# Kernel optimization log

Hardware: AMD Instinct MI355X
Metric: run time of the kernel (lower is better)

## Reference

```python
import jax, jax.numpy as jnp
import numpy as np

KER = 3          # CausalPool1d kernel
PAD_VAL = 1e-8   # left-pad value
K = 3            # harmonic_num
H = 4200         # rows of integral matrix
F = 321          # frequency bins


def setup_inputs() -> dict:
    key = jax.random.key(0)
    k1, k2, k3 = jax.random.split(key, 3)
    mag = jax.random.uniform(k1, (8, 2, F, 1000), dtype=jnp.float32)          # B,C,F,T (magnitude >= 0)
    integral_m = jax.random.normal(k2, (H, F), dtype=jnp.float32)             # buffer integral_m (squeezed)
    harmonic_loc = jax.random.normal(k3, (H, F), dtype=jnp.float32)           # buffer harmonic_loc (squeezed)
    return {"mag": mag, "integral_m": integral_m, "harmonic_loc": harmonic_loc, "freq_dim": F}


def reference(mag, integral_m, harmonic_loc, freq_dim):
    # harmonic_nominee: (B,C,H,T) = integral_m @ mag
    nominee = jnp.einsum('hf,bcft->bcht', integral_m, mag)
    # topk over the H axis (torch dim=-2); lax.top_k works on last axis -> move H last
    _, pos = jax.lax.top_k(jnp.moveaxis(nominee, 2, -1), K)  # (B,C,T,K), descending like torch
    pos = jnp.moveaxis(pos, -1, 2).astype(jnp.float32)       # (B,C,K,T)
    # CausalPool1d: left-pad (KER-1) with 1e-8, avg over window KER, stride 1 (vectorized over K)
    xp = jnp.pad(pos, ((0, 0), (0, 0), (0, 0), (KER - 1, 0)), constant_values=PAD_VAL)
    T = pos.shape[-1]
    choose = ((xp[..., 0:T] + xp[..., 1:T + 1] + xp[..., 2:T + 2]) / KER).astype(jnp.int32)  # (B,C,K,T)
    # gather harmonic_loc rows and accumulate over the K harmonics
    gathered = harmonic_loc[choose]          # (B,C,K,T,F)
    summed = gathered.sum(axis=2)            # (B,C,T,F)
    # (B,C,F,T) threshold mask, matching torch's (x > 0).float()
    out = (jnp.swapaxes(summed, -1, -2) > 0).astype(jnp.float32)
    return out
```

## Files before the change

### kernel.cpp

```cpp
#include <hip/hip_runtime.h>
#include <math.h>

#define F_DIM 321
#define H_DIM 4200
#define T_DIM 1000
#define NBC   16
#define KTOP  3
#define PADV  1e-8f

#define BM 128
#define BN 128
#define BK 16
#define LDA 16
#define LDB 128
#define NHT 33
#define NKT 20

typedef float v4f __attribute__((ext_vector_type(4)));
typedef __attribute__((address_space(3))) uint32_t lds_u32;
typedef const __attribute__((address_space(1))) uint32_t glb_u32;

__device__ __forceinline__ void ins3(float v, int i,
                                     float& v0, float& v1, float& v2,
                                     int& i0, int& i1, int& i2) {
  if (v > v0)      { v2 = v1; i2 = i1; v1 = v0; i1 = i0; v0 = v; i0 = i; }
  else if (v > v1) { v2 = v1; i2 = i1; v1 = v;  i1 = i; }
  else if (v > v2) { v2 = v;  i2 = i; }
}

__global__ __launch_bounds__(256)
void hi_k1_gemm_top3(const float* __restrict__ mag,
                     const float* __restrict__ im,
                     float* __restrict__ wv, int* __restrict__ wi,
                     int nsplit) {
  const int tid = threadIdx.x;
  const int tx = tid & 15;
  const int ty = tid >> 4;
  const int wv_ = tid >> 6;
  const int lam = tid & 63;
  const int t0 = blockIdx.x * BN;
  const int bc = blockIdx.y;
  const int sp = blockIdx.z;
  const int ht_begin = (sp * NHT) / nsplit;
  const int ht_end   = ((sp + 1) * NHT) / nsplit;
  const int nht = ht_end - ht_begin;
  const int NT = nht * NKT;
  const int row0 = ty * 8;
  const int xsw = (ty & 3) << 2;

  __shared__ __align__(16) float As[2][BM * LDA];
  __shared__ __align__(16) float Bs[2][BK * LDB];
  __shared__ float mv[4 * BN * KTOP];
  __shared__ int   mi[4 * BN * KTOP];

  const float* magbc = mag + (size_t)bc * F_DIM * T_DIM;

  auto stageA = [&](int buf, int nh0, int nk0) {
#pragma unroll
    for (int i = 0; i < 8; ++i) {
      int row = wv_ * 32 + i * 4 + (lam >> 4);
      int gh = nh0 + row;
      gh = (gh < H_DIM) ? gh : (H_DIM - 1);
      int key = ((row >> 3) & 3) << 2;
      const float* src = im + (size_t)gh * F_DIM + nk0 + ((lam & 15) ^ key);
      __builtin_amdgcn_global_load_lds(
          (glb_u32*)src,
          (lds_u32*)&As[buf][(wv_ * 32 + i * 4) * LDA], 4, 0, 0);
    }
  };
  auto stageB = [&](int buf, int nk0) {
#pragma unroll
    for (int i = 0; i < 2; ++i) {
      int kr = wv_ * 4 + i * 2 + (lam >> 5);
      const float* src = magbc + (size_t)(nk0 + kr) * T_DIM + t0 + (lam & 31) * 4;
      __builtin_amdgcn_global_load_lds(
          (glb_u32*)src,
          (lds_u32*)&Bs[buf][(wv_ * 4 + i * 2) * LDB], 16, 0, 0);
    }
  };
  auto nh0_of = [&](int i) { return (ht_begin + i / NKT) * BM; };
  auto nk0_of = [&](int i) { return (i % NKT) * BK; };

  float gv0 = -INFINITY, gv1 = -INFINITY, gv2 = -INFINITY;
  int   gi0 = 0, gi1 = 0, gi2 = 0;

  stageA(0, nh0_of(0), nk0_of(0)); stageB(0, nk0_of(0));
  stageA(1, nh0_of(1), nk0_of(1)); stageB(1, nk0_of(1));
  asm volatile("s_waitcnt vmcnt(10)" ::: "memory");
  __builtin_amdgcn_s_barrier();
  __builtin_amdgcn_sched_barrier(0);

  int cur = 0;
  for (int ht = 0; ht < nht; ++ht) {
    const int h0 = (ht_begin + ht) * BM;
    float acc[8][8];
#pragma unroll
    for (int r = 0; r < 8; ++r)
#pragma unroll
      for (int c = 0; c < 8; ++c) acc[r][c] = 0.f;

    for (int kt = 0; kt < NKT; ++kt) {
      const int i = ht * NKT + kt;

#pragma unroll 1
      for (int g = 0; g < 4; ++g) {
        v4f Bv[8];
#pragma unroll
        for (int kk = 0; kk < 4; ++kk) {
          Bv[kk * 2]     = *(const v4f*)(&Bs[cur][(g * 4 + kk) * LDB + tx * 4]);
          Bv[kk * 2 + 1] = *(const v4f*)(&Bs[cur][(g * 4 + kk) * LDB + 64 + tx * 4]);
        }
#pragma unroll
        for (int r = 0; r < 8; ++r) {
          const v4f Ar = *(const v4f*)(&As[cur][(row0 + r) * LDA + ((g * 4) ^ xsw)]);
#pragma unroll
          for (int kk = 0; kk < 4; ++kk)
#pragma unroll
            for (int c = 0; c < 4; ++c) {
              acc[r][c]     = fmaf(Ar[kk], Bv[kk * 2][c],     acc[r][c]);
              acc[r][c + 4] = fmaf(Ar[kk], Bv[kk * 2 + 1][c], acc[r][c + 4]);
            }
        }
      }

      asm volatile("" ::: "memory");
      __builtin_amdgcn_s_barrier();
      __builtin_amdgcn_sched_barrier(0);

      if (i + 2 < NT) {
        stageA(cur, nh0_of(i + 2), nk0_of(i + 2));
        stageB(cur, nk0_of(i + 2));
        asm volatile("s_waitcnt vmcnt(10)" ::: "memory");
      } else {
        asm volatile("s_waitcnt vmcnt(0)" ::: "memory");
      }
      asm volatile("" ::: "memory");
      __builtin_amdgcn_s_barrier();
      __builtin_amdgcn_sched_barrier(0);
      cur ^= 1;
    }

    {
      float bt[8];
#pragma unroll
      for (int c = 0; c < 8; ++c) {
        int gt = t0 + ((c < 4) ? (tx * 4 + c) : (64 + tx * 4 + c - 4));
        bt[c] = (gt < T_DIM) ? magbc[(size_t)(F_DIM - 1) * T_DIM + gt] : 0.f;
      }
#pragma unroll
      for (int r = 0; r < 8; ++r) {
        int gh = h0 + row0 + r;
        float a = (gh < H_DIM) ? im[(size_t)gh * F_DIM + (F_DIM - 1)] : 0.f;
#pragma unroll
        for (int c = 0; c < 8; ++c) acc[r][c] = fmaf(a, bt[c], acc[r][c]);
      }
    }

#pragma unroll
    for (int c = 0; c < 8; ++c) {
      const int col = (c < 4) ? (tx * 4 + c) : (64 + tx * 4 + c - 4);
      float v0 = -INFINITY, v1 = -INFINITY, v2 = -INFINITY;
      int   i0 = 0, i1 = 0, i2 = 0;
#pragma unroll
      for (int r = 0; r < 8; ++r) {
        int gh = h0 + row0 + r;
        float v = (gh < H_DIM) ? acc[r][c] : -INFINITY;
        ins3(v, gh, v0, v1, v2, i0, i1, i2);
      }
#pragma unroll
      for (int s = 0; s < 2; ++s) {
        const int off = 16 << s;
        float ov0 = __shfl_down(v0, off);
        float ov1 = __shfl_down(v1, off);
        float ov2 = __shfl_down(v2, off);
        int   oi0 = __shfl_down(i0, off);
        int   oi1 = __shfl_down(i1, off);
        int   oi2 = __shfl_down(i2, off);
        ins3(ov0, oi0, v0, v1, v2, i0, i1, i2);
        ins3(ov1, oi1, v0, v1, v2, i0, i1, i2);
        ins3(ov2, oi2, v0, v1, v2, i0, i1, i2);
      }
      if ((ty & 3) == 0) {
        mv[(wv_ * BN + col) * 3 + 0] = v0;
        mv[(wv_ * BN + col) * 3 + 1] = v1;
        mv[(wv_ * BN + col) * 3 + 2] = v2;
        mi[(wv_ * BN + col) * 3 + 0] = i0;
        mi[(wv_ * BN + col) * 3 + 1] = i1;
        mi[(wv_ * BN + col) * 3 + 2] = i2;
      }
    }
    __syncthreads();
    if (tid < BN) {
#pragma unroll
      for (int w = 0; w < 4; ++w)
#pragma unroll
        for (int j = 0; j < 3; ++j) {
          float v = mv[(w * BN + tid) * 3 + j];
          int   i = mi[(w * BN + tid) * 3 + j];
          ins3(v, i, gv0, gv1, gv2, gi0, gi1, gi2);
        }
    }
    __syncthreads();
  }

  if (tid < BN) {
    int t = t0 + tid;
    if (t < T_DIM) {
      size_t base = ((size_t)(bc * nsplit + sp) * KTOP) * T_DIM + t;
      wv[base]             = gv0;
      wv[base + T_DIM]     = gv1;
      wv[base + 2 * T_DIM] = gv2;
      wi[base]             = gi0;
      wi[base + T_DIM]     = gi1;
      wi[base + 2 * T_DIM] = gi2;
    }
  }
}

__global__ __launch_bounds__(256, 4)
void hi_k3_pool_gather(const float* __restrict__ wv, const int* __restrict__ wi,
                       const float* __restrict__ hl, float* __restrict__ out,
                       int nsplit) {
  const int tid = threadIdx.x;
  const int t0 = blockIdx.x * 64;
  const int bc = blockIdx.y;

  __shared__ float pos_lds[66 * KTOP];
  __shared__ int   rows[64 * KTOP];
  __shared__ float S[64 * 65];

  if (tid < 66) {
    int t = t0 - 2 + tid;
    float p0 = PADV, p1 = PADV, p2 = PADV;
    if (t >= 0 && t < T_DIM) {
      float v0 = -INFINITY, v1 = -INFINITY, v2 = -INFINITY;
      int i0 = 0, i1 = 0, i2 = 0;
      for (int sp = 0; sp < nsplit; ++sp)
        for (int j = 0; j < KTOP; ++j) {
          size_t idx = ((size_t)(bc * nsplit + sp) * KTOP + j) * T_DIM + t;
          ins3(wv[idx], wi[idx], v0, v1, v2, i0, i1, i2);
        }
      p0 = (float)i0; p1 = (float)i1; p2 = (float)i2;
    }
    pos_lds[tid * KTOP + 0] = p0;
    pos_lds[tid * KTOP + 1] = p1;
    pos_lds[tid * KTOP + 2] = p2;
  }
  __syncthreads();
  if (tid < 64) {
#pragma unroll
    for (int k = 0; k < KTOP; ++k) {
      float s = (pos_lds[tid * KTOP + k] + pos_lds[(tid + 1) * KTOP + k])
                + pos_lds[(tid + 2) * KTOP + k];
      rows[tid * KTOP + k] = (int)(s / 3.0f);
    }
  }
  __syncthreads();

  const int w = tid >> 6, lane = tid & 63;
  for (int fc = 0; fc < 6; ++fc) {
    const int f0 = fc * 64;
    for (int i = 0; i < 16; ++i) {
      int tl = w * 16 + i;
      int r0 = rows[tl * KTOP + 0];
      int r1 = rows[tl * KTOP + 1];
      int r2 = rows[tl * KTOP + 2];
      int f = f0 + lane;
      float s = 0.f;
      if (f < F_DIM)
        s = (hl[(size_t)r0 * F_DIM + f] + hl[(size_t)r1 * F_DIM + f])
            + hl[(size_t)r2 * F_DIM + f];
      S[tl * 65 + lane] = s;
    }
    __syncthreads();
#pragma unroll
    for (int i = 0; i < 16; ++i) {
      int e = tid + 256 * i;
      int fl = e >> 6, tl = e & 63;
      int f = f0 + fl, t = t0 + tl;
      if (f < F_DIM && t < T_DIM)
        out[((size_t)bc * F_DIM + f) * T_DIM + t] = (S[tl * 65 + fl] > 0.f) ? 1.f : 0.f;
    }
    __syncthreads();
  }
}

extern "C" void kernel_launch(void* const* d_in, const int* in_sizes, int n_in,
                              void* d_out, int out_size, void* d_ws, size_t ws_size,
                              hipStream_t stream) {
  const float* mag = (const float*)d_in[0];
  const float* im  = (const float*)d_in[1];
  const float* hl  = (const float*)d_in[2];
  float* out = (float*)d_out;

  int nsplit = (ws_size >= (size_t)NBC * 8 * KTOP * T_DIM * 8) ? 8 : 4;
  float* wv = (float*)d_ws;
  int*   wi = (int*)d_ws + (size_t)NBC * nsplit * KTOP * T_DIM;

  dim3 g1((T_DIM + BN - 1) / BN, NBC, nsplit);
  hipLaunchKernelGGL(hi_k1_gemm_top3, g1, dim3(256), 0, stream, mag, im, wv, wi, nsplit);

  dim3 g3((T_DIM + 63) / 64, NBC);
  hipLaunchKernelGGL(hi_k3_pool_gather, g3, dim3(256), 0, stream, wv, wi, hl, out, nsplit);
}
```

Baseline: 1.026 ms.

## Restructure top-3 GEMM to stream integral rows via scalar loads with wider column tiles

Each block now handles 32 rows of integral_m and 256 time columns, and each wave owns 8 rows. The A operand is no longer staged through LDS: each wave reads its rows with wave-uniform (readfirstlane) addresses, so they can become scalar loads feeding the FMAs directly. Only the mag tile is double-buffered through LDS, and the top-3 reduction drops its cross-lane shuffles because each lane already covers all rows of its columns. The H split now goes up to 32 when the workspace allows, which adds more partial results for the second kernel to merge. The change relies on scalar-cache hit rates and on whether unaligned scalar loads are efficient.

```diff
diff --git a/kernel.cpp b/kernel.cpp
--- a/kernel.cpp
+++ b/kernel.cpp
@@ -8,13 +8,12 @@
 #define KTOP  3
 #define PADV  1e-8f
 
-#define BM 128
-#define BN 128
+#define BM 32
+#define BN 256
 #define BK 16
-#define LDA 16
-#define LDB 128
-#define NHT 33
+#define NRT 132
 #define NKT 20
+#define NTT 4
 
 typedef float v4f __attribute__((ext_vector_type(4)));
 typedef __attribute__((address_space(3))) uint32_t lds_u32;
@@ -33,104 +32,88 @@
                      const float* __restrict__ im,
                      float* __restrict__ wv, int* __restrict__ wi,
                      int nsplit) {
-  const int tid = threadIdx.x;
-  const int tx = tid & 15;
-  const int ty = tid >> 4;
-  const int wv_ = tid >> 6;
-  const int lam = tid & 63;
+  const int tid  = threadIdx.x;
+  const int lane = tid & 63;
+  const int w    = tid >> 6;
   const int t0 = blockIdx.x * BN;
   const int bc = blockIdx.y;
   const int sp = blockIdx.z;
-  const int ht_begin = (sp * NHT) / nsplit;
-  const int ht_end   = ((sp + 1) * NHT) / nsplit;
-  const int nht = ht_end - ht_begin;
-  const int NT = nht * NKT;
-  const int row0 = ty * 8;
-  const int xsw = (ty & 3) << 2;
-
-  __shared__ __align__(16) float As[2][BM * LDA];
-  __shared__ __align__(16) float Bs[2][BK * LDB];
-  __shared__ float mv[4 * BN * KTOP];
-  __shared__ int   mi[4 * BN * KTOP];
+  const int rt_begin = (sp * NRT) / nsplit;
+  const int rt_end   = ((sp + 1) * NRT) / nsplit;
+
+  __shared__ __align__(16) float Bs[2][BK * BN];
+  float* mv = (float*)&Bs[0][0];
+  int*   mi = (int*)(&Bs[0][0] + 4 * BN * KTOP);
 
   const float* magbc = mag + (size_t)bc * F_DIM * T_DIM;
 
-  auto stageA = [&](int buf, int nh0, int nk0) {
-#pragma unroll
-    for (int i = 0; i < 8; ++i) {
-      int row = wv_ * 32 + i * 4 + (lam >> 4);
-      int gh = nh0 + row;
-      gh = (gh < H_DIM) ? gh : (H_DIM - 1);
-      int key = ((row >> 3) & 3) << 2;
-      const float* src = im + (size_t)gh * F_DIM + nk0 + ((lam & 15) ^ key);
+  auto stageB = [&](int buf, int k0) {
+#pragma unroll
+    for (int i = 0; i < 4; ++i) {
+      int kr = w * 4 + i;
+      const float* src = magbc + (size_t)(k0 + kr) * T_DIM + t0 + lane * 4;
       __builtin_amdgcn_global_load_lds(
-          (glb_u32*)src,
-          (lds_u32*)&As[buf][(wv_ * 32 + i * 4) * LDA], 4, 0, 0);
+          (glb_u32*)src, (lds_u32*)&Bs[buf][kr * BN], 16, 0, 0);
     }
   };
-  auto stageB = [&](int buf, int nk0) {
-#pragma unroll
-    for (int i = 0; i < 2; ++i) {
-      int kr = wv_ * 4 + i * 2 + (lam >> 5);
-      const float* src = magbc + (size_t)(nk0 + kr) * T_DIM + t0 + (lam & 31) * 4;
-      __builtin_amdgcn_global_load_lds(
-          (glb_u32*)src,
-          (lds_u32*)&Bs[buf][(wv_ * 4 + i * 2) * LDB], 16, 0, 0);
-    }
-  };
-  auto nh0_of = [&](int i) { return (ht_begin + i / NKT) * BM; };
-  auto nk0_of = [&](int i) { return (i % NKT) * BK; };
 
   float gv0 = -INFINITY, gv1 = -INFINITY, gv2 = -INFINITY;
   int   gi0 = 0, gi1 = 0, gi2 = 0;
 
-  stageA(0, nh0_of(0), nk0_of(0)); stageB(0, nk0_of(0));
-  stageA(1, nh0_of(1), nk0_of(1)); stageB(1, nk0_of(1));
-  asm volatile("s_waitcnt vmcnt(10)" ::: "memory");
-  __builtin_amdgcn_s_barrier();
-  __builtin_amdgcn_sched_barrier(0);
-
-  int cur = 0;
-  for (int ht = 0; ht < nht; ++ht) {
-    const int h0 = (ht_begin + ht) * BM;
-    float acc[8][8];
+  for (int rt = rt_begin; rt < rt_end; ++rt) {
+    const int h0 = rt * BM;
+    int ab[8];
+#pragma unroll
+    for (int r = 0; r < 8; ++r) {
+      int gh = h0 + w * 8 + r;
+      if (gh >= H_DIM) gh = H_DIM - 1;
+      ab[r] = __builtin_amdgcn_readfirstlane(gh * F_DIM);
+    }
+
+    float acc[8][4];
 #pragma unroll
     for (int r = 0; r < 8; ++r)
 #pragma unroll
-      for (int c = 0; c < 8; ++c) acc[r][c] = 0.f;
-
+      for (int c = 0; c < 4; ++c) acc[r][c] = 0.f;
+
+    stageB(0, 0);
+    stageB(1, BK);
+    asm volatile("s_waitcnt vmcnt(4)" ::: "memory");
+    __builtin_amdgcn_s_barrier();
+    __builtin_amdgcn_sched_barrier(0);
+
+    int cur = 0;
     for (int kt = 0; kt < NKT; ++kt) {
-      const int i = ht * NKT + kt;
-
-#pragma unroll 1
+      const int k0 = kt * BK;
+#pragma unroll 2
       for (int g = 0; g < 4; ++g) {
-        v4f Bv[8];
-#pragma unroll
-        for (int kk = 0; kk < 4; ++kk) {
-          Bv[kk * 2]     = *(const v4f*)(&Bs[cur][(g * 4 + kk) * LDB + tx * 4]);
-          Bv[kk * 2 + 1] = *(const v4f*)(&Bs[cur][(g * 4 + kk) * LDB + 64 + tx * 4]);
-        }
-#pragma unroll
-        for (int r = 0; r < 8; ++r) {
-          const v4f Ar = *(const v4f*)(&As[cur][(row0 + r) * LDA + ((g * 4) ^ xsw)]);
-#pragma unroll
-          for (int kk = 0; kk < 4; ++kk)
-#pragma unroll
-            for (int c = 0; c < 4; ++c) {
-              acc[r][c]     = fmaf(Ar[kk], Bv[kk * 2][c],     acc[r][c]);
-              acc[r][c + 4] = fmaf(Ar[kk], Bv[kk * 2 + 1][c], acc[r][c + 4]);
-            }
-        }
+        const int kk0 = k0 + g * 4;
+        float a[8][4];
+#pragma unroll
+        for (int r = 0; r < 8; ++r)
+#pragma unroll
+          for (int q = 0; q < 4; ++q)
+            a[r][q] = im[ab[r] + kk0 + q];
+        v4f Bv[4];
+#pragma unroll
+        for (int q = 0; q < 4; ++q)
+          Bv[q] = *(const v4f*)(&Bs[cur][(g * 4 + q) * BN + lane * 4]);
+#pragma unroll
+        for (int r = 0; r < 8; ++r)
+#pragma unroll
+          for (int q = 0; q < 4; ++q)
+#pragma unroll
+            for (int c = 0; c < 4; ++c)
+              acc[r][c] = fmaf(a[r][q], Bv[q][c], acc[r][c]);
       }
 
       asm volatile("" ::: "memory");
       __builtin_amdgcn_s_barrier();
       __builtin_amdgcn_sched_barrier(0);
 
-      if (i + 2 < NT) {
-        stageA(cur, nh0_of(i + 2), nk0_of(i + 2));
-        stageB(cur, nk0_of(i + 2));
-        asm volatile("s_waitcnt vmcnt(10)" ::: "memory");
+      if (kt + 2 < NKT) {
+        stageB(cur, (kt + 2) * BK);
+        asm volatile("s_waitcnt vmcnt(4)" ::: "memory");
       } else {
         asm volatile("s_waitcnt vmcnt(0)" ::: "memory");
       }
@@ -141,69 +124,54 @@
     }
 
     {
-      float bt[8];
-#pragma unroll
-      for (int c = 0; c < 8; ++c) {
-        int gt = t0 + ((c < 4) ? (tx * 4 + c) : (64 + tx * 4 + c - 4));
+      float bt[4];
+#pragma unroll
+      for (int c = 0; c < 4; ++c) {
+        int gt = t0 + lane * 4 + c;
         bt[c] = (gt < T_DIM) ? magbc[(size_t)(F_DIM - 1) * T_DIM + gt] : 0.f;
       }
 #pragma unroll
       for (int r = 0; r < 8; ++r) {
-        int gh = h0 + row0 + r;
-        float a = (gh < H_DIM) ? im[(size_t)gh * F_DIM + (F_DIM - 1)] : 0.f;
-#pragma unroll
-        for (int c = 0; c < 8; ++c) acc[r][c] = fmaf(a, bt[c], acc[r][c]);
-      }
-    }
-
-#pragma unroll
-    for (int c = 0; c < 8; ++c) {
-      const int col = (c < 4) ? (tx * 4 + c) : (64 + tx * 4 + c - 4);
+        float av = im[ab[r] + (F_DIM - 1)];
+#pragma unroll
+        for (int c = 0; c < 4; ++c) acc[r][c] = fmaf(av, bt[c], acc[r][c]);
+      }
+    }
+
+#pragma unroll
+    for (int c = 0; c < 4; ++c) {
+      const int col = lane * 4 + c;
       float v0 = -INFINITY, v1 = -INFINITY, v2 = -INFINITY;
       int   i0 = 0, i1 = 0, i2 = 0;
 #pragma unroll
       for (int r = 0; r < 8; ++r) {
-        int gh = h0 + row0 + r;
+        int gh = h0 + w * 8 + r;
         float v = (gh < H_DIM) ? acc[r][c] : -INFINITY;
         ins3(v, gh, v0, v1, v2, i0, i1, i2);
       }
-#pragma unroll
-      for (int s = 0; s < 2; ++s) {
-        const int off = 16 << s;
-        float ov0 = __shfl_down(v0, off);
-        float ov1 = __shfl_down(v1, off);
-        float ov2 = __shfl_down(v2, off);
-        int   oi0 = __shfl_down(i0, off);
-        int   oi1 = __shfl_down(i1, off);
-        int   oi2 = __shfl_down(i2, off);
-        ins3(ov0, oi0, v0, v1, v2, i0, i1, i2);
-        ins3(ov1, oi1, v0, v1, v2, i0, i1, i2);
-        ins3(ov2, oi2, v0, v1, v2, i0, i1, i2);
-      }
-      if ((ty & 3) == 0) {
-        mv[(wv_ * BN + col) * 3 + 0] = v0;
-        mv[(wv_ * BN + col) * 3 + 1] = v1;
-        mv[(wv_ * BN + col) * 3 + 2] = v2;
-        mi[(wv_ * BN + col) * 3 + 0] = i0;
-        mi[(wv_ * BN + col) * 3 + 1] = i1;
-        mi[(wv_ * BN + col) * 3 + 2] = i2;
-      }
-    }
-    __syncthreads();
-    if (tid < BN) {
-#pragma unroll
-      for (int w = 0; w < 4; ++w)
+      mv[(w * BN + col) * 3 + 0] = v0;
+      mv[(w * BN + col) * 3 + 1] = v1;
+      mv[(w * BN + col) * 3 + 2] = v2;
+      mi[(w * BN + col) * 3 + 0] = i0;
+      mi[(w * BN + col) * 3 + 1] = i1;
+      mi[(w * BN + col) * 3 + 2] = i2;
+    }
+    __syncthreads();
+    {
+      const int col = tid;
+#pragma unroll
+      for (int ww = 0; ww < 4; ++ww)
 #pragma unroll
         for (int j = 0; j < 3; ++j) {
-          float v = mv[(w * BN + tid) * 3 + j];
-          int   i = mi[(w * BN + tid) * 3 + j];
+          float v = mv[(ww * BN + col) * 3 + j];
+          int   i = mi[(ww * BN + col) * 3 + j];
           ins3(v, i, gv0, gv1, gv2, gi0, gi1, gi2);
         }
     }
     __syncthreads();
   }
 
-  if (tid < BN) {
+  {
     int t = t0 + tid;
     if (t < T_DIM) {
       size_t base = ((size_t)(bc * nsplit + sp) * KTOP) * T_DIM + t;
@@ -293,11 +261,13 @@
   const float* hl  = (const float*)d_in[2];
   float* out = (float*)d_out;
 
-  int nsplit = (ws_size >= (size_t)NBC * 8 * KTOP * T_DIM * 8) ? 8 : 4;
+  int nsplit = 8;
+  if (ws_size >= (size_t)NBC * 32 * KTOP * T_DIM * 8) nsplit = 32;
+  else if (ws_size >= (size_t)NBC * 16 * KTOP * T_DIM * 8) nsplit = 16;
   float* wv = (float*)d_ws;
   int*   wi = (int*)d_ws + (size_t)NBC * nsplit * KTOP * T_DIM;
 
-  dim3 g1((T_DIM + BN - 1) / BN, NBC, nsplit);
+  dim3 g1(NTT, NBC, nsplit);
   hipLaunchKernelGGL(hi_k1_gemm_top3, g1, dim3(256), 0, stream, mag, im, wv, wi, nsplit);
 
   dim3 g3((T_DIM + 63) / 64, NBC);
```

Result: faster. 960.3 us (-6.4%).
